# Kernel tuning notes

Measured on AMD Instinct MI355X. Metric: run time of the kernel, lower is better.

## Reference

```python
import jax, jax.numpy as jnp
import numpy as np

N, A, D_IN, H, S = 4096, 256, 39, 50, 8


def setup_inputs() -> dict:
    key = jax.random.key(0)
    ks = jax.random.split(key, 8)
    sc1 = 1.0 / np.sqrt(D_IN)
    sc2 = 1.0 / np.sqrt(H)
    return {
        "desc": jax.random.normal(ks[0], (N, A, D_IN), dtype=jnp.float32),
        "numbers": jax.random.randint(ks[1], (A,), 0, S),
        "W1": jax.random.normal(ks[2], (S, D_IN, H), dtype=jnp.float32) * sc1,
        "b1": jax.random.normal(ks[3], (S, H), dtype=jnp.float32) * sc1,
        "W2": jax.random.normal(ks[4], (S, H, H), dtype=jnp.float32) * sc2,
        "b2": jax.random.normal(ks[5], (S, H), dtype=jnp.float32) * sc2,
        "W3": jax.random.normal(ks[6], (S, H, 1), dtype=jnp.float32) * sc2,
        "b3": jax.random.normal(ks[7], (S, 1), dtype=jnp.float32) * sc2,
    }


def reference(desc, numbers, W1, b1, W2, b2, W3, b3):
    # Species-routed per-atom MLP dispatch, vectorized by gathering each
    # atom's expert parameters (replaces the Python loop over ModuleDict).
    w1 = W1[numbers]            # [A, D_IN, H]
    w2 = W2[numbers]            # [A, H, H]
    w3 = W3[numbers]            # [A, H, 1]
    h = jax.nn.silu(jnp.einsum('nad,adh->nah', desc, w1) + b1[numbers])
    h = jax.nn.silu(jnp.einsum('nah,ahk->nak', h, w2) + b2[numbers])
    out = jnp.einsum('nah,aho->nao', h, w3) + b3[numbers]
    return out[..., 0]          # [N, A], matches tc.cat(temp, axis=1)
```

## Files before the change

### kernel.cpp

```cpp
#include <hip/hip_runtime.h>
#include <hip/hip_bf16.h>
#include <cstring>


#define NN    4096
#define AA    256
#define DIN   39
#define HH    50
#define ATILE 4
#define NTILE 64
#define XSTR  56
#define WFS   (2 * 2 * 4 * 64 * 8)

typedef __attribute__((ext_vector_type(8))) short bf16x8;
typedef __attribute__((ext_vector_type(4))) float f32x4;

__device__ __forceinline__ float fast_silu(float x) {
    return x * __builtin_amdgcn_rcpf(1.0f + __expf(-x));
}
__device__ __forceinline__ unsigned pack_bf2(float a, float b) {
    __hip_bfloat162 h = __float22bfloat162_rn(float2{a, b});
    unsigned u; memcpy(&u, &h, 4); return u;
}
__device__ __forceinline__ unsigned short bf16b(float a) {
    __hip_bfloat16 h = __float2bfloat16(a);
    unsigned short u; memcpy(&u, &h, 2); return u;
}

__global__ __launch_bounds__(256) void prep_weights(
    const float* __restrict__ W1, const float* __restrict__ b1,
    const float* __restrict__ W2, const float* __restrict__ b2,
    const float* __restrict__ W3, const float* __restrict__ b3,
    unsigned short* __restrict__ Wf, float* __restrict__ Bp)
{
    const int s = blockIdx.x >> 3;
    const int c = blockIdx.x & 7;
    const int t = threadIdx.x;
    const float* __restrict__ w1g = W1 + s * (DIN * HH);
    const float* __restrict__ w2g = W2 + s * (HH * HH);
    unsigned* __restrict__ outw = (unsigned*)(Wf + (size_t)s * WFS);

    #pragma unroll
    for (int i = 0; i < 2; ++i) {
        const int d    = c * 512 + i * 256 + t;
        const int j2   = d & 3;
        const int lane = (d >> 2) & 63;
        const int mt   = (d >> 8) & 3;
        const int ks   = (d >> 10) & 1;
        const int L    = (d >> 11) & 1;
        const int col  = 16 * mt + (lane & 15);
        const int k0   = ks * 32 + 8 * (lane >> 4) + 2 * j2;
        const int k1   = k0 + 1;
        float v0 = 0.f, v1 = 0.f;
        if (col < HH) {
            if (L == 0) {
                if (k0 < DIN) v0 = w1g[k0 * HH + col];
                if (k1 < DIN) v1 = w1g[k1 * HH + col];
            } else {
                if (k0 < HH)  v0 = w2g[k0 * HH + col];
                if (k1 < HH)  v1 = w2g[k1 * HH + col];
            }
        }
        outw[d] = pack_bf2(v0, v1);
    }
    if (c == 0 && t < 64) {
        float* bp = Bp + s * 256;
        const bool v = t < HH;
        bp[t]       = v ? b1[s * HH + t] : 0.0f;
        bp[64 + t]  = v ? b2[s * HH + t] : 0.0f;
        bp[128 + t] = v ? W3[s * HH + t] : 0.0f;
        bp[192 + t] = b3[s];
    }
}

__global__ __launch_bounds__(256, 4) void atomic_mlp_mfma(
    const float* __restrict__ desc,
    const int*   __restrict__ numbers,
    const unsigned short* __restrict__ Wf,
    const float* __restrict__ Bp,
    float*       __restrict__ out)
{
    __shared__ unsigned short Xb[ATILE * NTILE * XSTR + 8];
    __shared__ float          Ob[ATILE * NTILE];

    const int a0 = blockIdx.x * ATILE;
    const int n0 = blockIdx.y * NTILE;
    const int t  = threadIdx.x;

    #pragma unroll
    for (int i = 0; i < 10; ++i) {
        const int idx = t + 256 * i;
        if (idx < NTILE * 39) {
            const int seg = idx / 39;
            const int off = idx - 39 * seg;
            const float4 v = *(const float4*)(desc +
                ((size_t)(n0 + seg) * AA + a0) * DIN + off * 4);
            const int f0 = off * 4;
            #pragma unroll
            for (int j = 0; j < 4; ++j) {
                const int f  = f0 + j;
                const int at = f / 39;
                const int d  = f - 39 * at;
                Xb[(at * NTILE + seg) * XSTR + d] = bf16b(((const float*)&v)[j]);
            }
        }
    }
    Xb[t * XSTR + 39] = 0;
    *(uint4*)&Xb[t * XSTR + 40] = uint4{0u, 0u, 0u, 0u};
    *(uint4*)&Xb[t * XSTR + 48] = uint4{0u, 0u, 0u, 0u};
    if (t == 0) *(uint4*)&Xb[ATILE * NTILE * XSTR] = uint4{0u, 0u, 0u, 0u};

    const int lane = t & 63;
    const int lg   = lane >> 4;
    const int lr   = lane & 15;
    const int wid  = t >> 6;
    const int wbase = wid * NTILE;

    const int sw = __builtin_amdgcn_readfirstlane(numbers[a0 + wid]);
    const unsigned short* __restrict__ wfs = Wf + (size_t)sw * WFS;

    bf16x8 w1f[2][4], w2f[2][4];
    #pragma unroll
    for (int ks = 0; ks < 2; ++ks)
        #pragma unroll
        for (int mt = 0; mt < 4; ++mt) {
            w1f[ks][mt] = *(const bf16x8*)&wfs[((ks * 4 + mt) * 64 + lane) * 8];
            w2f[ks][mt] = *(const bf16x8*)&wfs[((8 + ks * 4 + mt) * 64 + lane) * 8];
        }

    const float* __restrict__ bp = Bp + sw * 256;
    const float bias3 = bp[192];

    __syncthreads();

    #pragma unroll
    for (int nt = 0; nt < 4; ++nt) {
        const int row = wbase + 16 * nt + lr;
        bf16x8 xf0 = *(const bf16x8*)&Xb[row * XSTR + 8 * lg];
        bf16x8 xf1 = *(const bf16x8*)&Xb[row * XSTR + 32 + 8 * lg];
        #pragma unroll
        for (int mt = 0; mt < 4; ++mt) {
            f32x4 cAcc = f32x4{0.f, 0.f, 0.f, 0.f};
            cAcc = __builtin_amdgcn_mfma_f32_16x16x32_bf16(w1f[0][mt], xf0, cAcc, 0, 0, 0);
            cAcc = __builtin_amdgcn_mfma_f32_16x16x32_bf16(w1f[1][mt], xf1, cAcc, 0, 0, 0);
            const float4 b1q = *(const float4*)&bp[16 * mt + 4 * lg];
            const unsigned u0 = pack_bf2(fast_silu(cAcc[0] + b1q.x),
                                         fast_silu(cAcc[1] + b1q.y));
            const unsigned u1 = pack_bf2(fast_silu(cAcc[2] + b1q.z),
                                         fast_silu(cAcc[3] + b1q.w));
            if (mt < 3 || lg < 2) {
                uint2 uu; uu.x = u0; uu.y = u1;
                *(uint2*)&Xb[row * XSTR + 16 * mt + 4 * lg] = uu;
            }
        }
    }

    #pragma unroll
    for (int nt = 0; nt < 4; ++nt) {
        const int row = wbase + 16 * nt + lr;
        bf16x8 hf0 = *(const bf16x8*)&Xb[row * XSTR + 8 * lg];
        bf16x8 hf1 = *(const bf16x8*)&Xb[row * XSTR + 32 + 8 * lg];
        float p = 0.f;
        #pragma unroll
        for (int mt = 0; mt < 4; ++mt) {
            f32x4 cAcc = f32x4{0.f, 0.f, 0.f, 0.f};
            cAcc = __builtin_amdgcn_mfma_f32_16x16x32_bf16(w2f[0][mt], hf0, cAcc, 0, 0, 0);
            cAcc = __builtin_amdgcn_mfma_f32_16x16x32_bf16(w2f[1][mt], hf1, cAcc, 0, 0, 0);
            const float4 b2q = *(const float4*)&bp[64 + 16 * mt + 4 * lg];
            const float4 w3q = *(const float4*)&bp[128 + 16 * mt + 4 * lg];
            p += fast_silu(cAcc[0] + b2q.x) * w3q.x;
            p += fast_silu(cAcc[1] + b2q.y) * w3q.y;
            p += fast_silu(cAcc[2] + b2q.z) * w3q.z;
            p += fast_silu(cAcc[3] + b2q.w) * w3q.w;
        }
        p += __shfl_xor(p, 16);
        p += __shfl_xor(p, 32);
        if (lg == 0) Ob[wbase + 16 * nt + lr] = p + bias3;
    }

    __syncthreads();

    if (t < NTILE) {
        float4 o;
        o.x = Ob[0 * NTILE + t];
        o.y = Ob[1 * NTILE + t];
        o.z = Ob[2 * NTILE + t];
        o.w = Ob[3 * NTILE + t];
        *(float4*)&out[(size_t)(n0 + t) * AA + a0] = o;
    }
}

extern "C" void kernel_launch(void* const* d_in, const int* in_sizes, int n_in,
                              void* d_out, int out_size, void* d_ws, size_t ws_size,
                              hipStream_t stream) {
    const float* desc    = (const float*)d_in[0];
    const int*   numbers = (const int*)  d_in[1];
    const float* W1      = (const float*)d_in[2];
    const float* b1      = (const float*)d_in[3];
    const float* W2      = (const float*)d_in[4];
    const float* b2      = (const float*)d_in[5];
    const float* W3      = (const float*)d_in[6];
    const float* b3      = (const float*)d_in[7];
    float*       out     = (float*)d_out;

    unsigned short* Wf = (unsigned short*)d_ws;
    float*          Bp = (float*)((char*)d_ws + 8 * WFS * 2);

    hipLaunchKernelGGL(prep_weights, dim3(64), dim3(256), 0, stream,
                       W1, b1, W2, b2, W3, b3, Wf, Bp);

    dim3 grid(AA / ATILE, NN / NTILE);
    hipLaunchKernelGGL(atomic_mlp_mfma, grid, dim3(256), 0, stream,
                       desc, numbers, Wf, Bp, out);
}
```

Measured before the change: 75.66 us.

## Load descriptors directly into MFMA fragments, bypassing LDS staging

The descriptor tile is no longer staged through shared memory with a block-wide barrier. Instead each wave reads its atom's 39-float rows straight from global memory with unaligned vector loads and converts them in registers into the bf16 MFMA operand layout. Layer-2 weights and all bias vectors are now loaded per layer and pinned in registers with empty asm statements. The hidden buffer stride is widened to 72 so the padded columns can be written without a guard. This removes LDS scatter stores and one barrier, at the cost of less coalesced, strided global loads spread across the four waves and an extra overlapping load to cover the row tail.

```diff
diff --git a/kernel.cpp b/kernel.cpp
--- a/kernel.cpp
+++ b/kernel.cpp
@@ -9,11 +9,12 @@
 #define HH    50
 #define ATILE 4
 #define NTILE 64
-#define XSTR  56
+#define XSTR  72
 #define WFS   (2 * 2 * 4 * 64 * 8)
 
 typedef __attribute__((ext_vector_type(8))) short bf16x8;
 typedef __attribute__((ext_vector_type(4))) float f32x4;
+typedef float f32x4u __attribute__((ext_vector_type(4), aligned(4)));
 
 __device__ __forceinline__ float fast_silu(float x) {
     return x * __builtin_amdgcn_rcpf(1.0f + __expf(-x));
@@ -22,9 +23,13 @@
     __hip_bfloat162 h = __float22bfloat162_rn(float2{a, b});
     unsigned u; memcpy(&u, &h, 4); return u;
 }
-__device__ __forceinline__ unsigned short bf16b(float a) {
-    __hip_bfloat16 h = __float2bfloat16(a);
-    unsigned short u; memcpy(&u, &h, 2); return u;
+__device__ __forceinline__ bf16x8 cvt8(f32x4u a, f32x4u b) {
+    unsigned u[4];
+    u[0] = pack_bf2(a[0], a[1]);
+    u[1] = pack_bf2(a[2], a[3]);
+    u[2] = pack_bf2(b[0], b[1]);
+    u[3] = pack_bf2(b[2], b[3]);
+    bf16x8 r; memcpy(&r, u, 16); return r;
 }
 
 __global__ __launch_bounds__(256) void prep_weights(
@@ -80,36 +85,12 @@
     const float* __restrict__ Bp,
     float*       __restrict__ out)
 {
-    __shared__ unsigned short Xb[ATILE * NTILE * XSTR + 8];
+    __shared__ unsigned short Hb[ATILE * NTILE * XSTR];
     __shared__ float          Ob[ATILE * NTILE];
 
     const int a0 = blockIdx.x * ATILE;
     const int n0 = blockIdx.y * NTILE;
     const int t  = threadIdx.x;
-
-    #pragma unroll
-    for (int i = 0; i < 10; ++i) {
-        const int idx = t + 256 * i;
-        if (idx < NTILE * 39) {
-            const int seg = idx / 39;
-            const int off = idx - 39 * seg;
-            const float4 v = *(const float4*)(desc +
-                ((size_t)(n0 + seg) * AA + a0) * DIN + off * 4);
-            const int f0 = off * 4;
-            #pragma unroll
-            for (int j = 0; j < 4; ++j) {
-                const int f  = f0 + j;
-                const int at = f / 39;
-                const int d  = f - 39 * at;
-                Xb[(at * NTILE + seg) * XSTR + d] = bf16b(((const float*)&v)[j]);
-            }
-        }
-    }
-    Xb[t * XSTR + 39] = 0;
-    *(uint4*)&Xb[t * XSTR + 40] = uint4{0u, 0u, 0u, 0u};
-    *(uint4*)&Xb[t * XSTR + 48] = uint4{0u, 0u, 0u, 0u};
-    if (t == 0) *(uint4*)&Xb[ATILE * NTILE * XSTR] = uint4{0u, 0u, 0u, 0u};
-
     const int lane = t & 63;
     const int lg   = lane >> 4;
     const int lr   = lane & 15;
@@ -118,64 +99,96 @@
 
     const int sw = __builtin_amdgcn_readfirstlane(numbers[a0 + wid]);
     const unsigned short* __restrict__ wfs = Wf + (size_t)sw * WFS;
-
-    bf16x8 w1f[2][4], w2f[2][4];
-    #pragma unroll
-    for (int ks = 0; ks < 2; ++ks)
+    const float* __restrict__ bp = Bp + sw * 256;
+
+    bf16x8 w1f[2][4];
+    #pragma unroll
+    for (int ks = 0; ks < 2; ++ks)
+        #pragma unroll
+        for (int mt = 0; mt < 4; ++mt)
+            w1f[ks][mt] = *(const bf16x8*)&wfs[((ks * 4 + mt) * 64 + lane) * 8];
+    f32x4 b1q[4];
+    #pragma unroll
+    for (int mt = 0; mt < 4; ++mt)
+        b1q[mt] = *(const f32x4*)&bp[16 * mt + 4 * lg];
+    #pragma unroll
+    for (int ks = 0; ks < 2; ++ks)
+        #pragma unroll
+        for (int mt = 0; mt < 4; ++mt)
+            asm volatile("" : "+v"(w1f[ks][mt]));
+    #pragma unroll
+    for (int mt = 0; mt < 4; ++mt) asm volatile("" : "+v"(b1q[mt]));
+
+    const float bias3 = bp[192];
+
+    const size_t arow = (size_t)(a0 + wid) * DIN;
+    #pragma unroll
+    for (int nt = 0; nt < 4; ++nt) {
+        const size_t rbase = (size_t)(n0 + 16 * nt + lr) * (AA * DIN) + arow;
+        const f32x4u xa = *(const f32x4u*)(desc + rbase + 8 * lg);
+        const f32x4u xb = *(const f32x4u*)(desc + rbase + 8 * lg + 4);
+        const f32x4u xc = *(const f32x4u*)(desc + rbase + 32);
+        const f32x4u xv = *(const f32x4u*)(desc + rbase + 35);
+        f32x4u xd;
+        xd[0] = xv[1]; xd[1] = xv[2]; xd[2] = xv[3]; xd[3] = xv[0];
+        const bf16x8 xf0 = cvt8(xa, xb);
+        const bf16x8 xf1 = cvt8(xc, xd);
         #pragma unroll
         for (int mt = 0; mt < 4; ++mt) {
-            w1f[ks][mt] = *(const bf16x8*)&wfs[((ks * 4 + mt) * 64 + lane) * 8];
+            f32x4 c = f32x4{0.f, 0.f, 0.f, 0.f};
+            c = __builtin_amdgcn_mfma_f32_16x16x32_bf16(w1f[0][mt], xf0, c, 0, 0, 0);
+            c = __builtin_amdgcn_mfma_f32_16x16x32_bf16(w1f[1][mt], xf1, c, 0, 0, 0);
+            const unsigned u0 = pack_bf2(fast_silu(c[0] + b1q[mt][0]),
+                                         fast_silu(c[1] + b1q[mt][1]));
+            const unsigned u1 = pack_bf2(fast_silu(c[2] + b1q[mt][2]),
+                                         fast_silu(c[3] + b1q[mt][3]));
+            uint2 uu; uu.x = u0; uu.y = u1;
+            *(uint2*)&Hb[(wbase + 16 * nt + lr) * XSTR + 16 * mt + 4 * lg] = uu;
+        }
+    }
+
+    bf16x8 w2f[2][4];
+    #pragma unroll
+    for (int ks = 0; ks < 2; ++ks)
+        #pragma unroll
+        for (int mt = 0; mt < 4; ++mt)
             w2f[ks][mt] = *(const bf16x8*)&wfs[((8 + ks * 4 + mt) * 64 + lane) * 8];
-        }
-
-    const float* __restrict__ bp = Bp + sw * 256;
-    const float bias3 = bp[192];
-
-    __syncthreads();
+    f32x4 b2q[4], w3q[4];
+    #pragma unroll
+    for (int mt = 0; mt < 4; ++mt) {
+        b2q[mt] = *(const f32x4*)&bp[64 + 16 * mt + 4 * lg];
+        w3q[mt] = *(const f32x4*)&bp[128 + 16 * mt + 4 * lg];
+    }
+    #pragma unroll
+    for (int ks = 0; ks < 2; ++ks)
+        #pragma unroll
+        for (int mt = 0; mt < 4; ++mt)
+            asm volatile("" : "+v"(w2f[ks][mt]));
+    #pragma unroll
+    for (int mt = 0; mt < 4; ++mt) {
+        asm volatile("" : "+v"(b2q[mt]));
+        asm volatile("" : "+v"(w3q[mt]));
+    }
 
     #pragma unroll
     for (int nt = 0; nt < 4; ++nt) {
         const int row = wbase + 16 * nt + lr;
-        bf16x8 xf0 = *(const bf16x8*)&Xb[row * XSTR + 8 * lg];
-        bf16x8 xf1 = *(const bf16x8*)&Xb[row * XSTR + 32 + 8 * lg];
+        const bf16x8 hf0 = *(const bf16x8*)&Hb[row * XSTR + 8 * lg];
+        const bf16x8 hf1 = *(const bf16x8*)&Hb[row * XSTR + 32 + 8 * lg];
+        float p = 0.f;
         #pragma unroll
         for (int mt = 0; mt < 4; ++mt) {
-            f32x4 cAcc = f32x4{0.f, 0.f, 0.f, 0.f};
-            cAcc = __builtin_amdgcn_mfma_f32_16x16x32_bf16(w1f[0][mt], xf0, cAcc, 0, 0, 0);
-            cAcc = __builtin_amdgcn_mfma_f32_16x16x32_bf16(w1f[1][mt], xf1, cAcc, 0, 0, 0);
-            const float4 b1q = *(const float4*)&bp[16 * mt + 4 * lg];
-            const unsigned u0 = pack_bf2(fast_silu(cAcc[0] + b1q.x),
-                                         fast_silu(cAcc[1] + b1q.y));
-            const unsigned u1 = pack_bf2(fast_silu(cAcc[2] + b1q.z),
-                                         fast_silu(cAcc[3] + b1q.w));
-            if (mt < 3 || lg < 2) {
-                uint2 uu; uu.x = u0; uu.y = u1;
-                *(uint2*)&Xb[row * XSTR + 16 * mt + 4 * lg] = uu;
-            }
-        }
-    }
-
-    #pragma unroll
-    for (int nt = 0; nt < 4; ++nt) {
-        const int row = wbase + 16 * nt + lr;
-        bf16x8 hf0 = *(const bf16x8*)&Xb[row * XSTR + 8 * lg];
-        bf16x8 hf1 = *(const bf16x8*)&Xb[row * XSTR + 32 + 8 * lg];
-        float p = 0.f;
-        #pragma unroll
-        for (int mt = 0; mt < 4; ++mt) {
-            f32x4 cAcc = f32x4{0.f, 0.f, 0.f, 0.f};
-            cAcc = __builtin_amdgcn_mfma_f32_16x16x32_bf16(w2f[0][mt], hf0, cAcc, 0, 0, 0);
-            cAcc = __builtin_amdgcn_mfma_f32_16x16x32_bf16(w2f[1][mt], hf1, cAcc, 0, 0, 0);
-            const float4 b2q = *(const float4*)&bp[64 + 16 * mt + 4 * lg];
-            const float4 w3q = *(const float4*)&bp[128 + 16 * mt + 4 * lg];
-            p += fast_silu(cAcc[0] + b2q.x) * w3q.x;
-            p += fast_silu(cAcc[1] + b2q.y) * w3q.y;
-            p += fast_silu(cAcc[2] + b2q.z) * w3q.z;
-            p += fast_silu(cAcc[3] + b2q.w) * w3q.w;
+            f32x4 c = f32x4{0.f, 0.f, 0.f, 0.f};
+            c = __builtin_amdgcn_mfma_f32_16x16x32_bf16(w2f[0][mt], hf0, c, 0, 0, 0);
+            c = __builtin_amdgcn_mfma_f32_16x16x32_bf16(w2f[1][mt], hf1, c, 0, 0, 0);
+            p += fast_silu(c[0] + b2q[mt][0]) * w3q[mt][0];
+            p += fast_silu(c[1] + b2q[mt][1]) * w3q[mt][1];
+            p += fast_silu(c[2] + b2q[mt][2]) * w3q[mt][2];
+            p += fast_silu(c[3] + b2q[mt][3]) * w3q[mt][3];
         }
         p += __shfl_xor(p, 16);
         p += __shfl_xor(p, 32);
-        if (lg == 0) Ob[wbase + 16 * nt + lr] = p + bias3;
+        if (lg == 0) Ob[row] = p + bias3;
     }
 
     __syncthreads();
```

New measurement: 65.42 us. -13.5%, faster.
